# Kernel optimization log

Hardware: AMD Instinct MI355X
Metric: run time of the kernel (lower is better)

Reference implementation:

```python
import jax, jax.numpy as jnp
import numpy as np

CMP_STRIDE, CMP_BLOCK = 16, 32
SEL_BLOCK, SEL_COUNT = 64, 16
WINDOW = 512
B, S, HQ, HKV, D = 1, 1536, 16, 2, 128


def setup_inputs() -> dict:
    key = jax.random.key(0)
    ks = jax.random.split(key, 10)
    f = lambda k_, sh, sc=1.0: jax.random.normal(k_, sh, jnp.float32) * sc
    return {
        "q": f(ks[0], (B * S, HQ, D)),
        "k": f(ks[1], (B * S, HKV, D)),
        "v": f(ks[2], (B * S, HKV, D)),
        "Wk": f(ks[3], (CMP_BLOCK * D, D), 0.02),
        "bk": jnp.zeros((D,), jnp.float32),
        "Wv": f(ks[4], (CMP_BLOCK * D, D), 0.02),
        "bv": jnp.zeros((D,), jnp.float32),
        "pek": f(ks[5], (CMP_BLOCK, D), 0.02),
        "pev": f(ks[6], (CMP_BLOCK, D), 0.02),
        "Wg": f(ks[7], (D, 3), 0.02),
        "bg": jnp.zeros((3,), jnp.float32),
        "cu_seqlens": jnp.array([0, S], jnp.int32),
        "max_seqlen": S,
    }


def _compress(x, W, b, pe):
    # x: [B,T,H,D] -> overlapping blocks (stride 16, len 32) -> learned linear per block
    Bb, T, H, Dd = x.shape
    Tc = (T - CMP_BLOCK) // CMP_STRIDE + 1
    idx = jnp.arange(Tc)[:, None] * CMP_STRIDE + jnp.arange(CMP_BLOCK)[None, :]
    blk = x[:, idx] + pe[None, None, :, None, :]          # [B,Tc,L,H,D] + intra-block pos emb
    blk = blk.transpose(0, 1, 3, 2, 4).reshape(Bb, Tc, H, CMP_BLOCK * Dd)
    return blk @ W + b                                    # [B,Tc,H,D]


def _msoftmax(logits, mask):
    # masked softmax; fully-masked rows produce zeros
    logits = jnp.where(mask, logits, jnp.finfo(logits.dtype).min)
    m = jnp.max(logits, -1, keepdims=True)
    e = jnp.exp(logits - m) * mask
    return e / jnp.maximum(e.sum(-1, keepdims=True), 1e-9)


def _forward(q, k, v, Wk, bk, Wv, bv, pek, pev, Wg, bg):
    scale = 1.0 / jnp.sqrt(jnp.float32(D))
    G = HQ // HKV
    qb = q.reshape(B, S, HQ, D)
    kb = k.reshape(B, S, HKV, D)
    vb = v.reshape(B, S, HKV, D)
    pos = jnp.arange(S)[:, None]

    # ---- stage 1: compressed-KV attention ----
    ck = _compress(kb, Wk, bk, pek)                        # [B,Tc,HKV,D]
    cv = _compress(vb, Wv, bv, pev)
    Tc = ck.shape[1]
    ckh = jnp.repeat(ck, G, axis=2)
    cvh = jnp.repeat(cv, G, axis=2)
    cl = jnp.einsum('bshd,bthd->bhst', qb, ckh) * scale    # [B,HQ,S,Tc]
    cmask = (jnp.arange(Tc)[None, :] * CMP_STRIDE + CMP_BLOCK - 1) <= pos  # block fully visible
    cp = _msoftmax(cl, cmask[None, None])
    cmp_o = jnp.einsum('bhst,bthd->bshd', cp, cvh)

    # ---- stage 2: pooled-score top-k block selection ----
    score = cp.reshape(B, HKV, G, S, Tc).sum(2)            # sum over GQA group -> [B,HKV,S,Tc]
    Kp = SEL_BLOCK // CMP_STRIDE + 1                       # AvgPool1d kernel = 5
    St = SEL_BLOCK // CMP_STRIDE                           # stride = 4
    P = CMP_BLOCK // CMP_STRIDE - 2                        # padding = 0
    n_out = -(-(Tc + 2 * P - Kp) // St) + 1                # ceil_mode=True
    widx = jnp.arange(n_out)[:, None] * St - P + jnp.arange(Kp)[None, :]
    inb = (widx >= 0) & (widx < Tc)
    cnt = ((widx >= -P) & (widx < Tc + P)).sum(-1)         # count_include_pad divisor
    gathered = jnp.where(inb[None, None, None], score[..., jnp.clip(widx, 0, Tc - 1)], 0.0)
    pooled = gathered.sum(-1) / cnt                        # [B,HKV,S,n_out]
    _, top_idx = jax.lax.top_k(pooled, SEL_COUNT)          # [B,HKV,S,SEL_COUNT]

    # ---- stage 3: block-sparse selected attention + sliding window ----
    n_kblk = S // SEL_BLOCK
    blk_sel = (top_idx[..., None] == jnp.arange(n_kblk)).any(-2)   # [B,HKV,S,n_kblk]
    key_blk = jnp.arange(S) // SEL_BLOCK
    causal = jnp.arange(S)[None, :] <= pos                 # [S,S]
    sel_mask = jnp.take(blk_sel, key_blk, axis=-1) & causal[None, None]
    sel_mask = jnp.repeat(sel_mask, G, axis=1)             # [B,HQ,S,S]
    win_mask = causal & (jnp.arange(S)[None, :] > pos - WINDOW)

    kh = jnp.repeat(kb, G, axis=2)
    vh = jnp.repeat(vb, G, axis=2)
    logits = jnp.einsum('bshd,buhd->bhsu', qb, kh) * scale # [B,HQ,S,S]
    sel_o = jnp.einsum('bhsu,buhd->bshd', _msoftmax(logits, sel_mask), vh)
    win_o = jnp.einsum('bhsu,buhd->bshd', _msoftmax(logits, win_mask[None, None]), vh)

    # ---- gated combine of three branches ----
    gate = jax.nn.sigmoid(jnp.einsum('bshd,de->bshe', qb, Wg) + bg)  # [B,S,HQ,3]
    o = gate[..., 0:1] * sel_o + gate[..., 1:2] * win_o + gate[..., 2:3] * cmp_o
    return o.reshape(-1, HQ, D)


def reference(q, k, v, Wk, bk, Wv, bv, pek, pev, Wg, bg, cu_seqlens, max_seqlen):
    return _forward(q, k, v, Wk, bk, Wv, bv, pek, pev, Wg, bg)
```

## Files before the change

### kernel.cpp

```cpp
#include <hip/hip_runtime.h>


#define S_LEN 1536
#define HQ    16
#define HKV   2
#define DH    128
#define TC    95
#define WIN   512
#define TQ    16
#define SCALE 0.08838834764831845f

typedef _Float16 f16;
typedef f16   f16x4 __attribute__((ext_vector_type(4)));
typedef f16   f16x8 __attribute__((ext_vector_type(8)));
typedef float f32x4 __attribute__((ext_vector_type(4)));

__device__ inline f16x8 cvt8(float4 A, float4 B) {
    f16x8 h;
    h[0]=(f16)A.x; h[1]=(f16)A.y; h[2]=(f16)A.z; h[3]=(f16)A.w;
    h[4]=(f16)B.x; h[5]=(f16)B.y; h[6]=(f16)B.z; h[7]=(f16)B.w;
    return h;
}
__device__ inline f16x8 cvt8s(float4 A, float4 B, float s) {
    f16x8 h;
    h[0]=(f16)(A.x*s); h[1]=(f16)(A.y*s); h[2]=(f16)(A.z*s); h[3]=(f16)(A.w*s);
    h[4]=(f16)(B.x*s); h[5]=(f16)(B.y*s); h[6]=(f16)(B.z*s); h[7]=(f16)(B.w*s);
    return h;
}

__global__ __launch_bounds__(256) void compress_init_kernel(
    const float* __restrict__ bk, const float* __restrict__ bv,
    float* __restrict__ ck, float* __restrict__ cv)
{
    int i = blockIdx.x * 256 + threadIdx.x;
    int which = i >= TC*HKV*DH;
    int j = i - which*(TC*HKV*DH);
    int d = j & 127;
    (which ? cv : ck)[j] = (which ? bv : bk)[d];
}

__global__ __launch_bounds__(256) void compress_partial_kernel(
    const float* __restrict__ kin, const float* __restrict__ vin,
    const float* __restrict__ Wk,  const float* __restrict__ Wv,
    const float* __restrict__ pek, const float* __restrict__ pev,
    float* __restrict__ ck, float* __restrict__ cv)
{
    const int t0    = blockIdx.x * 5;
    const int kv    = blockIdx.y >> 1;
    const int which = blockIdx.y & 1;
    const int kc    = blockIdx.z;
    const float* __restrict__ x  = which ? vin : kin;
    const float* __restrict__ W  = which ? Wv  : Wk;
    const float* __restrict__ pe = which ? pev : pek;
    float* __restrict__ outp     = which ? cv  : ck;
    const int tid = threadIdx.x;
    const int hh  = tid >> 7;
    const int d   = tid & 127;

    __shared__ float xs[2][5][128];
    __shared__ float racc[5][128];
    float acc[5] = {0.f, 0.f, 0.f, 0.f, 0.f};

    #pragma unroll
    for (int il = 0; il < 2; ++il) {
        const int l = kc*4 + hh*2 + il;
        float p = pe[l*DH + d];
        #pragma unroll
        for (int tt = 0; tt < 5; ++tt) {
            int row = (t0 + tt)*16 + l;
            xs[hh][tt][d] = x[(row*HKV + kv)*DH + d] + p;
        }
        __syncthreads();
        const float* wcol = W + l*DH*DH + d;
        #pragma unroll 8
        for (int dd = 0; dd < 128; ++dd) {
            float wv = wcol[dd*DH];
            #pragma unroll
            for (int tt = 0; tt < 5; ++tt) acc[tt] += xs[hh][tt][dd] * wv;
        }
        __syncthreads();
    }
    if (hh == 1) {
        #pragma unroll
        for (int tt = 0; tt < 5; ++tt) racc[tt][d] = acc[tt];
    }
    __syncthreads();
    if (hh == 0) {
        #pragma unroll
        for (int tt = 0; tt < 5; ++tt)
            atomicAdd(&outp[((t0 + tt)*HKV + kv)*DH + d], acc[tt] + racc[tt][d]);
    }
}

__global__ __launch_bounds__(256) void cmp_attn_mfma(
    const float* __restrict__ q, const float* __restrict__ ck,
    const float* __restrict__ cv, float* __restrict__ cmp_o,
    unsigned int* __restrict__ blk_mask)
{
    const int s0   = blockIdx.x * 8;
    const int kv   = blockIdx.y;
    const int tid  = threadIdx.x;
    const int w    = tid >> 6;
    const int lane = tid & 63;
    const int quad = lane >> 4;
    const int l4   = lane & 15;

    __shared__ __align__(16) char BUF[52736];
    f16* __restrict__ CKH = (f16*)BUF;
    f16* __restrict__ CKL = (f16*)(BUF + 26112);
    f16* __restrict__ CVR = (f16*)BUF;
    f16* __restrict__ CVT = (f16*)(BUF + 26112);
    f16*   __restrict__ Pw = (f16*)BUF + w*1664;
    float* __restrict__ SC = (float*)(BUF + 13312);
    float* __restrict__ PO = (float*)(BUF + 16384);

    #pragma unroll
    for (int i = 0; i < 6; ++i) {
        int idx = i*256 + tid;
        int row = idx >> 4, cg = idx & 15;
        float4 A = make_float4(0.f,0.f,0.f,0.f), B = A;
        if (row < TC) {
            const float* src = ck + ((size_t)(row*HKV + kv))*DH + cg*8;
            A = *(const float4*)src; B = *(const float4*)(src + 4);
        }
        f16x8 h = cvt8(A, B);
        f16x8 l;
        l[0]=(f16)(A.x-(float)h[0]); l[1]=(f16)(A.y-(float)h[1]);
        l[2]=(f16)(A.z-(float)h[2]); l[3]=(f16)(A.w-(float)h[3]);
        l[4]=(f16)(B.x-(float)h[4]); l[5]=(f16)(B.y-(float)h[5]);
        l[6]=(f16)(B.z-(float)h[6]); l[7]=(f16)(B.w-(float)h[7]);
        *(f16x8*)&CKH[row*136 + cg*8] = h;
        *(f16x8*)&CKL[row*136 + cg*8] = l;
    }

    const int qrow_local = w*16 + l4;
    const int sA = s0 + (qrow_local >> 3);
    const int hA = qrow_local & 7;
    f16x8 aqh[4], aql[4];
    {
        const float* qrow = q + ((size_t)(sA*HQ + kv*8 + hA))*DH;
        #pragma unroll
        for (int ks = 0; ks < 4; ++ks) {
            float4 A = *(const float4*)(qrow + ks*32 + quad*8);
            float4 B = *(const float4*)(qrow + ks*32 + quad*8 + 4);
            A.x*=SCALE; A.y*=SCALE; A.z*=SCALE; A.w*=SCALE;
            B.x*=SCALE; B.y*=SCALE; B.z*=SCALE; B.w*=SCALE;
            f16x8 h = cvt8(A, B);
            f16x8 l;
            l[0]=(f16)(A.x-(float)h[0]); l[1]=(f16)(A.y-(float)h[1]);
            l[2]=(f16)(A.z-(float)h[2]); l[3]=(f16)(A.w-(float)h[3]);
            l[4]=(f16)(B.x-(float)h[4]); l[5]=(f16)(B.y-(float)h[5]);
            l[6]=(f16)(B.z-(float)h[6]); l[7]=(f16)(B.w-(float)h[7]);
            aqh[ks] = h; aql[ks] = l;
        }
    }
    __syncthreads();

    f32x4 sc[6];
    #pragma unroll
    for (int nt = 0; nt < 6; ++nt) {
        sc[nt] = (f32x4){0.f,0.f,0.f,0.f};
        #pragma unroll
        for (int ks = 0; ks < 4; ++ks) {
            f16x8 bh = *(const f16x8*)&CKH[(nt*16 + l4)*136 + ks*32 + quad*8];
            f16x8 bl = *(const f16x8*)&CKL[(nt*16 + l4)*136 + ks*32 + quad*8];
            sc[nt] = __builtin_amdgcn_mfma_f32_16x16x32_f16(aqh[ks], bh, sc[nt], 0, 0, 0);
            sc[nt] = __builtin_amdgcn_mfma_f32_16x16x32_f16(aql[ks], bh, sc[nt], 0, 0, 0);
            sc[nt] = __builtin_amdgcn_mfma_f32_16x16x32_f16(aqh[ks], bl, sc[nt], 0, 0, 0);
        }
    }
    __syncthreads();

    #pragma unroll
    for (int i = 0; i < 6; ++i) {
        int idx = i*256 + tid;
        int row = idx >> 4, cg = idx & 15;
        float4 A = make_float4(0.f,0.f,0.f,0.f), B = A;
        if (row < TC) {
            const float* src = cv + ((size_t)(row*HKV + kv))*DH + cg*8;
            A = *(const float4*)src; B = *(const float4*)(src + 4);
        }
        *(f16x8*)&CVR[row*136 + cg*8] = cvt8(A, B);
    }
    __syncthreads();
    #pragma unroll
    for (int i = 0; i < 6; ++i) {
        int idx = i*256 + tid;
        int d = idx & 127, tc = idx >> 7;
        f16x8 h;
        #pragma unroll
        for (int j = 0; j < 8; ++j) h[j] = CVR[(tc*8 + j)*136 + d];
        *(f16x8*)&CVT[d*104 + tc*8] = h;
    }
    __syncthreads();

    const int s_q = s0 + 2*w + (quad >> 1);
    const int nv  = (s_q >= 31) ? (((s_q - 31) >> 4) + 1) : 0;
    bool valid[6];
    #pragma unroll
    for (int nt = 0; nt < 6; ++nt) valid[nt] = (nt*16 + l4) < nv;

    float pn[6][4];
    float lsum[4];
    #pragma unroll
    for (int r = 0; r < 4; ++r) {
        float m = -3.4e38f;
        #pragma unroll
        for (int nt = 0; nt < 6; ++nt) m = fmaxf(m, valid[nt] ? sc[nt][r] : -3.4e38f);
        #pragma unroll
        for (int off = 1; off < 16; off <<= 1) m = fmaxf(m, __shfl_xor(m, off));
        float s = 0.f;
        #pragma unroll
        for (int nt = 0; nt < 6; ++nt) {
            float e = valid[nt] ? __expf(sc[nt][r] - m) : 0.f;
            pn[nt][r] = e;
            s += e;
        }
        #pragma unroll
        for (int off = 1; off < 16; off <<= 1) s += __shfl_xor(s, off);
        const float inv = 1.f / fmaxf(s, 1e-9f);
        #pragma unroll
        for (int nt = 0; nt < 6; ++nt) pn[nt][r] *= inv;
        lsum[r] = s;
    }
    (void)lsum;

    #pragma unroll
    for (int nt = 0; nt < 6; ++nt) {
        #pragma unroll
        for (int r = 0; r < 4; ++r)
            Pw[(quad*4 + r)*104 + nt*16 + l4] = (f16)pn[nt][r];
        float scq = pn[nt][0] + pn[nt][1] + pn[nt][2] + pn[nt][3];
        scq += __shfl_xor(scq, 16);
        if ((quad & 1) == 0)
            SC[(w*2 + (quad >> 1))*96 + nt*16 + l4] = scq;
    }

    {
        int qi = lane >> 5;
        int o  = lane & 31;
        bool sel = false;
        if (o < 24) {
            float acc = 0.f, cnt = 0.f;
            #pragma unroll
            for (int j = 0; j < 5; ++j) {
                int wd = o*4 + j;
                if (wd < TC) { acc += SC[(w*2 + qi)*96 + wd]; cnt += 1.f; }
            }
            PO[(w*2 + qi)*24 + o] = acc / cnt;
        }
        if (o < 24) {
            float pvv = PO[(w*2 + qi)*24 + o];
            int rank = 0;
            #pragma unroll
            for (int j = 0; j < 24; ++j) {
                float pj = PO[(w*2 + qi)*24 + j];
                rank += ((pj > pvv) || (pj == pvv && j < o)) ? 1 : 0;
            }
            sel = rank < 16;
        }
        unsigned long long b = __ballot(sel);
        if (lane == 0) {
            blk_mask[kv*S_LEN + s0 + 2*w]     = (unsigned int)(b & 0xFFFFFFull);
            blk_mask[kv*S_LEN + s0 + 2*w + 1] = (unsigned int)((b >> 32) & 0xFFFFFFull);
        }
    }

    f32x4 O[8];
    #pragma unroll
    for (int nf = 0; nf < 8; ++nf) O[nf] = (f32x4){0.f,0.f,0.f,0.f};
    #pragma unroll
    for (int ks2 = 0; ks2 < 3; ++ks2) {
        f16x8 ap = *(const f16x8*)&Pw[l4*104 + ks2*32 + quad*8];
        #pragma unroll
        for (int nf = 0; nf < 8; ++nf) {
            f16x8 bv = *(const f16x8*)&CVT[(nf*16 + l4)*104 + ks2*32 + quad*8];
            O[nf] = __builtin_amdgcn_mfma_f32_16x16x32_f16(ap, bv, O[nf], 0, 0, 0);
        }
    }
    #pragma unroll
    for (int r = 0; r < 4; ++r) {
        const int h_r = (quad & 1)*4 + r;
        const size_t base = ((size_t)(s_q*HQ + kv*8 + h_r))*DH;
        #pragma unroll
        for (int nf = 0; nf < 8; ++nf)
            cmp_o[base + nf*16 + l4] = O[nf][r];
    }
}

__global__ __launch_bounds__(256, 2) void main_attn_split(
    const float* __restrict__ q, const float* __restrict__ kg,
    const float* __restrict__ vg,
    const unsigned int* __restrict__ blk_mask,
    float* __restrict__ po, float* __restrict__ ml,
    int nsplit)
{
    const int t0    = (S_LEN/TQ - 1 - blockIdx.x) * TQ;
    const int kv    = blockIdx.y;
    const int z     = blockIdx.z & 1;
    const int split = blockIdx.z >> 1;
    const int tid   = threadIdx.x;
    const int w     = tid >> 6;
    const int lane  = tid & 63;
    const int quad  = lane >> 4;
    const int l4    = lane & 15;
    const int head  = z*4 + w;

    __shared__ __align__(16) f16 Klds[64*136];
    __shared__ __align__(16) f16 Vt[128*72];
    __shared__ __align__(16) f16 Plds[4][16*72];
    f16* __restrict__ Pw = Plds[w];

    int srow[4]; unsigned selm[4];
    #pragma unroll
    for (int r = 0; r < 4; ++r) {
        srow[r] = t0 + quad*4 + r;
        selm[r] = blk_mask[kv*S_LEN + srow[r]];
    }
    unsigned um = 0;
    for (int i = 0; i < TQ; ++i) um |= blk_mask[kv*S_LEN + t0 + i];

    const int nkb = ((t0 + TQ - 1) >> 6) + 1;
    const int wlo_tile = t0 - WIN + 1;

    unsigned act_all = 0;
    for (int kb2 = 0; kb2 < nkb; ++kb2) {
        bool a = ((um >> kb2) & 1u) || ((kb2*64 + 63) >= wlo_tile);
        if (a) act_all |= (1u << kb2);
    }
    unsigned act = 0;
    {
        int ii = 0;
        for (unsigned t = act_all; t; t &= t - 1, ++ii)
            if (ii % nsplit == split) act |= (t & -t);
    }
    if (act == 0) {
        #pragma unroll
        for (int r = 0; r < 4; ++r) {
            const size_t rh = (size_t)srow[r]*HQ + kv*8 + head;
            const size_t bs = ((size_t)(split*2+0)*S_LEN*HQ + rh)*DH;
            const size_t bw = ((size_t)(split*2+1)*S_LEN*HQ + rh)*DH;
            #pragma unroll
            for (int nf = 0; nf < 8; ++nf) {
                po[bs + nf*16 + l4] = 0.f;
                po[bw + nf*16 + l4] = 0.f;
            }
            if (l4 == 0) {
                const size_t ms = ((size_t)(split*2+0)*S_LEN*HQ + rh)*2;
                const size_t mw = ((size_t)(split*2+1)*S_LEN*HQ + rh)*2;
                ml[ms+0] = -1e30f; ml[ms+1] = 0.f;
                ml[mw+0] = -1e30f; ml[mw+1] = 0.f;
            }
        }
        return;
    }

    f16x8 aq[4];
    {
        const float* qrow = q + ((size_t)(t0 + l4)*HQ + kv*8 + head)*DH;
        #pragma unroll
        for (int ks = 0; ks < 4; ++ks) {
            float4 A = *(const float4*)(qrow + ks*32 + quad*8);
            float4 B = *(const float4*)(qrow + ks*32 + quad*8 + 4);
            aq[ks] = cvt8s(A, B, SCALE);
        }
    }

    f32x4 o_s[8], o_w[8];
    #pragma unroll
    for (int nf = 0; nf < 8; ++nf) {
        o_s[nf] = (f32x4){0.f,0.f,0.f,0.f};
        o_w[nf] = (f32x4){0.f,0.f,0.f,0.f};
    }
    float m_s[4], l_s[4], m_w[4], l_w[4];
    #pragma unroll
    for (int r = 0; r < 4; ++r) { m_s[r]=-1e30f; l_s[r]=0.f; m_w[r]=-1e30f; l_w[r]=0.f; }

    int key_[4], cg_[4], vd_[4], vk_[4];
    #pragma unroll
    for (int i = 0; i < 4; ++i) {
        int idx = i*256 + tid;
        key_[i] = idx >> 4;  cg_[i] = idx & 15;
        vd_[i]  = idx & 127; vk_[i] = idx >> 7;
    }

    float4 pkA[4], pkB[4];
    float  pv[4][8];
    int kb = __builtin_ctz(act); act &= act - 1;
    #pragma unroll
    for (int i = 0; i < 4; ++i) {
        const float* sK = kg + ((size_t)(kb*64 + key_[i])*HKV + kv)*DH + cg_[i]*8;
        pkA[i] = *(const float4*)sK; pkB[i] = *(const float4*)(sK + 4);
        #pragma unroll
        for (int j = 0; j < 8; ++j)
            pv[i][j] = vg[((size_t)(kb*64 + vk_[i]*8 + j)*HKV + kv)*DH + vd_[i]];
    }

    while (true) {
        __syncthreads();
        #pragma unroll
        for (int i = 0; i < 4; ++i)
            *(f16x8*)&Klds[key_[i]*136 + cg_[i]*8] = cvt8(pkA[i], pkB[i]);
        #pragma unroll
        for (int i = 0; i < 4; ++i) {
            f16x8 h;
            #pragma unroll
            for (int j = 0; j < 8; ++j) h[j] = (f16)pv[i][j];
            *(f16x8*)&Vt[vd_[i]*72 + vk_[i]*8] = h;
        }
        __syncthreads();

        const int cur = kb;
        const bool more = (act != 0);
        if (more) {
            kb = __builtin_ctz(act); act &= act - 1;
            #pragma unroll
            for (int i = 0; i < 4; ++i) {
                const float* sK = kg + ((size_t)(kb*64 + key_[i])*HKV + kv)*DH + cg_[i]*8;
                pkA[i] = *(const float4*)sK; pkB[i] = *(const float4*)(sK + 4);
                #pragma unroll
                for (int j = 0; j < 8; ++j)
                    pv[i][j] = vg[((size_t)(kb*64 + vk_[i]*8 + j)*HKV + kv)*DH + vd_[i]];
            }
        }

        f32x4 sc[4];
        #pragma unroll
        for (int nt = 0; nt < 4; ++nt) {
            sc[nt] = (f32x4){0.f,0.f,0.f,0.f};
            #pragma unroll
            for (int ks = 0; ks < 4; ++ks) {
                f16x8 bk = *(const f16x8*)&Klds[(nt*16 + l4)*136 + ks*32 + quad*8];
                sc[nt] = __builtin_amdgcn_mfma_f32_16x16x32_f16(aq[ks], bk, sc[nt], 0, 0, 0);
            }
        }

        const int keyb = cur*64;
        const bool any_sel = (um >> cur) & 1u;
        const bool any_win = (keyb + 63) >= wlo_tile;
        if (any_sel) {
            float rmax[4] = {-1e30f,-1e30f,-1e30f,-1e30f};
            #pragma unroll
            for (int nt = 0; nt < 4; ++nt) {
                int key = keyb + nt*16 + l4;
                #pragma unroll
                for (int r = 0; r < 4; ++r) {
                    bool ok = (key <= srow[r]) && ((selm[r] >> cur) & 1u);
                    rmax[r] = fmaxf(rmax[r], ok ? sc[nt][r] : -1e30f);
                }
            }
            float alpha[4];
            #pragma unroll
            for (int r = 0; r < 4; ++r) {
                #pragma unroll
                for (int off = 1; off < 16; off <<= 1)
                    rmax[r] = fmaxf(rmax[r], __shfl_xor(rmax[r], off));
                float nm = fmaxf(m_s[r], rmax[r]);
                alpha[r] = __expf(m_s[r] - nm);
                m_s[r] = nm;
            }
            float rs[4] = {0.f,0.f,0.f,0.f};
            #pragma unroll
            for (int nt = 0; nt < 4; ++nt) {
                int key = keyb + nt*16 + l4;
                #pragma unroll
                for (int r = 0; r < 4; ++r) {
                    bool ok = (key <= srow[r]) && ((selm[r] >> cur) & 1u);
                    float p = ok ? __expf(sc[nt][r] - m_s[r]) : 0.f;
                    rs[r] += p;
                    Pw[(quad*4 + r)*72 + nt*16 + l4] = (f16)p;
                }
            }
            #pragma unroll
            for (int r = 0; r < 4; ++r) {
                #pragma unroll
                for (int off = 1; off < 16; off <<= 1) rs[r] += __shfl_xor(rs[r], off);
                l_s[r] = l_s[r]*alpha[r] + rs[r];
            }
            #pragma unroll
            for (int nf = 0; nf < 8; ++nf) {
                #pragma unroll
                for (int r = 0; r < 4; ++r) o_s[nf][r] *= alpha[r];
            }
            #pragma unroll
            for (int ks2 = 0; ks2 < 2; ++ks2) {
                f16x8 ap = *(const f16x8*)&Pw[l4*72 + ks2*32 + quad*8];
                #pragma unroll
                for (int nf = 0; nf < 8; ++nf) {
                    f16x8 bv = *(const f16x8*)&Vt[(nf*16 + l4)*72 + ks2*32 + quad*8];
                    o_s[nf] = __builtin_amdgcn_mfma_f32_16x16x32_f16(ap, bv, o_s[nf], 0, 0, 0);
                }
            }
        }
        if (any_win) {
            float rmax[4] = {-1e30f,-1e30f,-1e30f,-1e30f};
            #pragma unroll
            for (int nt = 0; nt < 4; ++nt) {
                int key = keyb + nt*16 + l4;
                #pragma unroll
                for (int r = 0; r < 4; ++r) {
                    bool ok = (key <= srow[r]) && (key > srow[r] - WIN);
                    rmax[r] = fmaxf(rmax[r], ok ? sc[nt][r] : -1e30f);
                }
            }
            float alpha[4];
            #pragma unroll
            for (int r = 0; r < 4; ++r) {
                #pragma unroll
                for (int off = 1; off < 16; off <<= 1)
                    rmax[r] = fmaxf(rmax[r], __shfl_xor(rmax[r], off));
                float nm = fmaxf(m_w[r], rmax[r]);
                alpha[r] = __expf(m_w[r] - nm);
                m_w[r] = nm;
            }
            float rs[4] = {0.f,0.f,0.f,0.f};
            #pragma unroll
            for (int nt = 0; nt < 4; ++nt) {
                int key = keyb + nt*16 + l4;
                #pragma unroll
                for (int r = 0; r < 4; ++r) {
                    bool ok = (key <= srow[r]) && (key > srow[r] - WIN);
                    float p = ok ? __expf(sc[nt][r] - m_w[r]) : 0.f;
                    rs[r] += p;
                    Pw[(quad*4 + r)*72 + nt*16 + l4] = (f16)p;
                }
            }
            #pragma unroll
            for (int r = 0; r < 4; ++r) {
                #pragma unroll
                for (int off = 1; off < 16; off <<= 1) rs[r] += __shfl_xor(rs[r], off);
                l_w[r] = l_w[r]*alpha[r] + rs[r];
            }
            #pragma unroll
            for (int nf = 0; nf < 8; ++nf) {
                #pragma unroll
                for (int r = 0; r < 4; ++r) o_w[nf][r] *= alpha[r];
            }
            #pragma unroll
            for (int ks2 = 0; ks2 < 2; ++ks2) {
                f16x8 ap = *(const f16x8*)&Pw[l4*72 + ks2*32 + quad*8];
                #pragma unroll
                for (int nf = 0; nf < 8; ++nf) {
                    f16x8 bv = *(const f16x8*)&Vt[(nf*16 + l4)*72 + ks2*32 + quad*8];
                    o_w[nf] = __builtin_amdgcn_mfma_f32_16x16x32_f16(ap, bv, o_w[nf], 0, 0, 0);
                }
            }
        }

        if (!more) break;
    }

    #pragma unroll
    for (int r = 0; r < 4; ++r) {
        const size_t rh = (size_t)srow[r]*HQ + kv*8 + head;
        const size_t bs = ((size_t)(split*2+0)*S_LEN*HQ + rh)*DH;
        const size_t bw = ((size_t)(split*2+1)*S_LEN*HQ + rh)*DH;
        #pragma unroll
        for (int nf = 0; nf < 8; ++nf) {
            po[bs + nf*16 + l4] = o_s[nf][r];
            po[bw + nf*16 + l4] = o_w[nf][r];
        }
        if (l4 == 0) {
            const size_t ms = ((size_t)(split*2+0)*S_LEN*HQ + rh)*2;
            const size_t mw = ((size_t)(split*2+1)*S_LEN*HQ + rh)*2;
            ml[ms+0] = m_s[r]; ml[ms+1] = l_s[r];
            ml[mw+0] = m_w[r]; ml[mw+1] = l_w[r];
        }
    }
}

__global__ __launch_bounds__(256) void combine_kernel(
    const float* __restrict__ q, const float* __restrict__ po,
    const float* __restrict__ ml, const float* __restrict__ Wg,
    const float* __restrict__ bg, float* __restrict__ out, int nsplit)
{
    const int unit = blockIdx.x * 4 + (threadIdx.x >> 6);
    const int lane = threadIdx.x & 63;
    const int row  = unit >> 4;
    const int h    = unit & 15;
    const size_t rh = (size_t)row*HQ + h;

    float p0 = 0.f, p1 = 0.f, p2 = 0.f;
    const float* qrow = q + rh*DH;
    #pragma unroll
    for (int t = 0; t < 2; ++t) {
        int d = t*64 + lane;
        float qv = qrow[d];
        p0 += qv*Wg[d*3+0]; p1 += qv*Wg[d*3+1]; p2 += qv*Wg[d*3+2];
    }
    #pragma unroll
    for (int off = 1; off < 64; off <<= 1) {
        p0 += __shfl_xor(p0, off);
        p1 += __shfl_xor(p1, off);
        p2 += __shfl_xor(p2, off);
    }
    const float g0 = 1.f/(1.f + __expf(-(p0 + bg[0])));
    const float g1 = 1.f/(1.f + __expf(-(p1 + bg[1])));
    const float g2 = 1.f/(1.f + __expf(-(p2 + bg[2])));

    float res0 = 0.f, res1 = 0.f;
    #pragma unroll
    for (int b = 0; b < 2; ++b) {
        float M = -1e30f;
        for (int s = 0; s < nsplit; ++s)
            M = fmaxf(M, ml[((size_t)(s*2+b)*S_LEN*HQ + rh)*2 + 0]);
        float L = 0.f, osum0 = 0.f, osum1 = 0.f;
        for (int s = 0; s < nsplit; ++s) {
            const size_t mlb = ((size_t)(s*2+b)*S_LEN*HQ + rh)*2;
            const float wgt = __expf(ml[mlb+0] - M);
            L += ml[mlb+1] * wgt;
            const size_t ob = ((size_t)(s*2+b)*S_LEN*HQ + rh)*DH;
            osum0 += po[ob + lane]      * wgt;
            osum1 += po[ob + 64 + lane] * wgt;
        }
        const float inv = 1.f / fmaxf(L, 1e-9f);
        const float g = b ? g1 : g0;
        res0 += g * osum0 * inv;
        res1 += g * osum1 * inv;
    }
    const size_t ob = rh*DH;
    out[ob + lane]      = res0 + g2*out[ob + lane];
    out[ob + 64 + lane] = res1 + g2*out[ob + 64 + lane];
}

__global__ __launch_bounds__(256, 2) void main_attn_mfma(
    const float* __restrict__ q, const float* __restrict__ kg,
    const float* __restrict__ vg, const float* cmp_o,
    const unsigned int* __restrict__ blk_mask,
    const float* __restrict__ Wg, const float* __restrict__ bg,
    float* out)
{
    const int t0   = (S_LEN/TQ - 1 - blockIdx.x) * TQ;
    const int kv   = blockIdx.y;
    const int z    = blockIdx.z;
    const int tid  = threadIdx.x;
    const int w    = tid >> 6;
    const int lane = tid & 63;
    const int quad = lane >> 4;
    const int l4   = lane & 15;
    const int head = z*4 + w;

    __shared__ __align__(16) f16 Klds[64*136];
    __shared__ __align__(16) f16 Vrow[64*136];
    __shared__ __align__(16) f16 Vt[128*72];
    __shared__ __align__(16) f16 Plds[4][16*72];
    f16* __restrict__ Pw = Plds[w];

    f16x8 aq[4];
    {
        const float* qrow = q + ((size_t)(t0 + l4)*HQ + kv*8 + head)*DH;
        #pragma unroll
        for (int ks = 0; ks < 4; ++ks) {
            float4 A = *(const float4*)(qrow + ks*32 + quad*8);
            float4 B = *(const float4*)(qrow + ks*32 + quad*8 + 4);
            aq[ks] = cvt8s(A, B, SCALE);
        }
    }

    int srow[4]; unsigned selm[4];
    #pragma unroll
    for (int r = 0; r < 4; ++r) {
        srow[r] = t0 + quad*4 + r;
        selm[r] = blk_mask[kv*S_LEN + srow[r]];
    }
    unsigned um = 0;
    for (int i = 0; i < TQ; ++i) um |= blk_mask[kv*S_LEN + t0 + i];

    f32x4 o_s[8], o_w[8];
    #pragma unroll
    for (int nf = 0; nf < 8; ++nf) {
        o_s[nf] = (f32x4){0.f,0.f,0.f,0.f};
        o_w[nf] = (f32x4){0.f,0.f,0.f,0.f};
    }
    float m_s[4], l_s[4], m_w[4], l_w[4];
    #pragma unroll
    for (int r = 0; r < 4; ++r) { m_s[r]=-1e30f; l_s[r]=0.f; m_w[r]=-1e30f; l_w[r]=0.f; }

    const int nkb = ((t0 + TQ - 1) >> 6) + 1;
    const int wlo_tile = t0 - WIN + 1;

    unsigned act = 0;
    for (int kb2 = 0; kb2 < nkb; ++kb2) {
        bool a = ((um >> kb2) & 1u) || ((kb2*64 + 63) >= wlo_tile);
        if (a) act |= (1u << kb2);
    }

    int key_[4], cg_[4];
    #pragma unroll
    for (int i = 0; i < 4; ++i) { int idx = i*256 + tid; key_[i] = idx >> 4; cg_[i] = idx & 15; }

    float4 pkA[4], pkB[4], pvA[4], pvB[4];
    int kb = __builtin_ctz(act); act &= act - 1;
    #pragma unroll
    for (int i = 0; i < 4; ++i) {
        const float* sK = kg + ((size_t)(kb*64 + key_[i])*HKV + kv)*DH + cg_[i]*8;
        const float* sV = vg + ((size_t)(kb*64 + key_[i])*HKV + kv)*DH + cg_[i]*8;
        pkA[i] = *(const float4*)sK; pkB[i] = *(const float4*)(sK + 4);
        pvA[i] = *(const float4*)sV; pvB[i] = *(const float4*)(sV + 4);
    }

    while (true) {
        __syncthreads();
        #pragma unroll
        for (int i = 0; i < 4; ++i) {
            *(f16x8*)&Klds[key_[i]*136 + cg_[i]*8] = cvt8(pkA[i], pkB[i]);
            *(f16x8*)&Vrow[key_[i]*136 + cg_[i]*8] = cvt8(pvA[i], pvB[i]);
        }
        __syncthreads();

        const int cur = kb;
        const bool more = (act != 0);
        if (more) {
            kb = __builtin_ctz(act); act &= act - 1;
            #pragma unroll
            for (int i = 0; i < 4; ++i) {
                const float* sK = kg + ((size_t)(kb*64 + key_[i])*HKV + kv)*DH + cg_[i]*8;
                const float* sV = vg + ((size_t)(kb*64 + key_[i])*HKV + kv)*DH + cg_[i]*8;
                pkA[i] = *(const float4*)sK; pkB[i] = *(const float4*)(sK + 4);
                pvA[i] = *(const float4*)sV; pvB[i] = *(const float4*)(sV + 4);
            }
        }

        #pragma unroll
        for (int i = 0; i < 4; ++i) {
            int idx = i*256 + tid;
            int d = idx & 127, kg8 = idx >> 7;
            f16x8 h;
            #pragma unroll
            for (int j = 0; j < 8; ++j) h[j] = Vrow[(kg8*8 + j)*136 + d];
            *(f16x8*)&Vt[d*72 + kg8*8] = h;
        }
        __syncthreads();

        f32x4 sc[4];
        #pragma unroll
        for (int nt = 0; nt < 4; ++nt) {
            sc[nt] = (f32x4){0.f,0.f,0.f,0.f};
            #pragma unroll
            for (int ks = 0; ks < 4; ++ks) {
                f16x8 bk = *(const f16x8*)&Klds[(nt*16 + l4)*136 + ks*32 + quad*8];
                sc[nt] = __builtin_amdgcn_mfma_f32_16x16x32_f16(aq[ks], bk, sc[nt], 0, 0, 0);
            }
        }

        const int keyb = cur*64;
        const bool any_sel = (um >> cur) & 1u;
        const bool any_win = (keyb + 63) >= wlo_tile;
        if (any_sel) {
            float rmax[4] = {-1e30f,-1e30f,-1e30f,-1e30f};
            #pragma unroll
            for (int nt = 0; nt < 4; ++nt) {
                int key = keyb + nt*16 + l4;
                #pragma unroll
                for (int r = 0; r < 4; ++r) {
                    bool ok = (key <= srow[r]) && ((selm[r] >> cur) & 1u);
                    rmax[r] = fmaxf(rmax[r], ok ? sc[nt][r] : -1e30f);
                }
            }
            float alpha[4];
            #pragma unroll
            for (int r = 0; r < 4; ++r) {
                #pragma unroll
                for (int off = 1; off < 16; off <<= 1)
                    rmax[r] = fmaxf(rmax[r], __shfl_xor(rmax[r], off));
                float nm = fmaxf(m_s[r], rmax[r]);
                alpha[r] = __expf(m_s[r] - nm);
                m_s[r] = nm;
            }
            float rs[4] = {0.f,0.f,0.f,0.f};
            #pragma unroll
            for (int nt = 0; nt < 4; ++nt) {
                int key = keyb + nt*16 + l4;
                #pragma unroll
                for (int r = 0; r < 4; ++r) {
                    bool ok = (key <= srow[r]) && ((selm[r] >> cur) & 1u);
                    float p = ok ? __expf(sc[nt][r] - m_s[r]) : 0.f;
                    rs[r] += p;
                    Pw[(quad*4 + r)*72 + nt*16 + l4] = (f16)p;
                }
            }
            #pragma unroll
            for (int r = 0; r < 4; ++r) {
                #pragma unroll
                for (int off = 1; off < 16; off <<= 1) rs[r] += __shfl_xor(rs[r], off);
                l_s[r] = l_s[r]*alpha[r] + rs[r];
            }
            #pragma unroll
            for (int nf = 0; nf < 8; ++nf) {
                #pragma unroll
                for (int r = 0; r < 4; ++r) o_s[nf][r] *= alpha[r];
            }
            #pragma unroll
            for (int ks2 = 0; ks2 < 2; ++ks2) {
                f16x8 ap = *(const f16x8*)&Pw[l4*72 + ks2*32 + quad*8];
                #pragma unroll
                for (int nf = 0; nf < 8; ++nf) {
                    f16x8 bv = *(const f16x8*)&Vt[(nf*16 + l4)*72 + ks2*32 + quad*8];
                    o_s[nf] = __builtin_amdgcn_mfma_f32_16x16x32_f16(ap, bv, o_s[nf], 0, 0, 0);
                }
            }
        }
        if (any_win) {
            float rmax[4] = {-1e30f,-1e30f,-1e30f,-1e30f};
            #pragma unroll
            for (int nt = 0; nt < 4; ++nt) {
                int key = keyb + nt*16 + l4;
                #pragma unroll
                for (int r = 0; r < 4; ++r) {
                    bool ok = (key <= srow[r]) && (key > srow[r] - WIN);
                    rmax[r] = fmaxf(rmax[r], ok ? sc[nt][r] : -1e30f);
                }
            }
            float alpha[4];
            #pragma unroll
            for (int r = 0; r < 4; ++r) {
                #pragma unroll
                for (int off = 1; off < 16; off <<= 1)
                    rmax[r] = fmaxf(rmax[r], __shfl_xor(rmax[r], off));
                float nm = fmaxf(m_w[r], rmax[r]);
                alpha[r] = __expf(m_w[r] - nm);
                m_w[r] = nm;
            }
            float rs[4] = {0.f,0.f,0.f,0.f};
            #pragma unroll
            for (int nt = 0; nt < 4; ++nt) {
                int key = keyb + nt*16 + l4;
                #pragma unroll
                for (int r = 0; r < 4; ++r) {
                    bool ok = (key <= srow[r]) && (key > srow[r] - WIN);
                    float p = ok ? __expf(sc[nt][r] - m_w[r]) : 0.f;
                    rs[r] += p;
                    Pw[(quad*4 + r)*72 + nt*16 + l4] = (f16)p;
                }
            }
            #pragma unroll
            for (int r = 0; r < 4; ++r) {
                #pragma unroll
                for (int off = 1; off < 16; off <<= 1) rs[r] += __shfl_xor(rs[r], off);
                l_w[r] = l_w[r]*alpha[r] + rs[r];
            }
            #pragma unroll
            for (int nf = 0; nf < 8; ++nf) {
                #pragma unroll
                for (int r = 0; r < 4; ++r) o_w[nf][r] *= alpha[r];
            }
            #pragma unroll
            for (int ks2 = 0; ks2 < 2; ++ks2) {
                f16x8 ap = *(const f16x8*)&Pw[l4*72 + ks2*32 + quad*8];
                #pragma unroll
                for (int nf = 0; nf < 8; ++nf) {
                    f16x8 bv = *(const f16x8*)&Vt[(nf*16 + l4)*72 + ks2*32 + quad*8];
                    o_w[nf] = __builtin_amdgcn_mfma_f32_16x16x32_f16(ap, bv, o_w[nf], 0, 0, 0);
                }
            }
        }

        if (!more) break;
    }

    float inv_s[4], inv_w[4];
    #pragma unroll
    for (int r = 0; r < 4; ++r) {
        inv_s[r] = 1.f / fmaxf(l_s[r], 1e-9f);
        inv_w[r] = 1.f / fmaxf(l_w[r], 1e-9f);
    }
    float gt[4][3];
    #pragma unroll
    for (int r = 0; r < 4; ++r) {
        float p0 = 0.f, p1 = 0.f, p2 = 0.f;
        const float* qrow = q + ((size_t)srow[r]*HQ + kv*8 + head)*DH + l4*8;
        #pragma unroll
        for (int j = 0; j < 8; ++j) {
            float qv = qrow[j];
            int d = l4*8 + j;
            p0 += qv * Wg[d*3 + 0];
            p1 += qv * Wg[d*3 + 1];
            p2 += qv * Wg[d*3 + 2];
        }
        #pragma unroll
        for (int off = 1; off < 16; off <<= 1) {
            p0 += __shfl_xor(p0, off);
            p1 += __shfl_xor(p1, off);
            p2 += __shfl_xor(p2, off);
        }
        gt[r][0] = 1.f/(1.f + __expf(-(p0 + bg[0])));
        gt[r][1] = 1.f/(1.f + __expf(-(p1 + bg[1])));
        gt[r][2] = 1.f/(1.f + __expf(-(p2 + bg[2])));
    }
    #pragma unroll
    for (int nf = 0; nf < 8; ++nf) {
        int d = nf*16 + l4;
        #pragma unroll
        for (int r = 0; r < 4; ++r) {
            size_t oi = ((size_t)srow[r]*HQ + kv*8 + head)*DH + d;
            float cm = cmp_o[oi];
            out[oi] = gt[r][0]*o_s[nf][r]*inv_s[r]
                    + gt[r][1]*o_w[nf][r]*inv_w[r]
                    + gt[r][2]*cm;
        }
    }
}

extern "C" void kernel_launch(void* const* d_in, const int* in_sizes, int n_in,
                              void* d_out, int out_size, void* d_ws, size_t ws_size,
                              hipStream_t stream) {
    const float* q   = (const float*)d_in[0];
    const float* k   = (const float*)d_in[1];
    const float* v   = (const float*)d_in[2];
    const float* Wk  = (const float*)d_in[3];
    const float* bk  = (const float*)d_in[4];
    const float* Wv  = (const float*)d_in[5];
    const float* bv  = (const float*)d_in[6];
    const float* pek = (const float*)d_in[7];
    const float* pev = (const float*)d_in[8];
    const float* Wg  = (const float*)d_in[9];
    const float* bg  = (const float*)d_in[10];
    float* out = (float*)d_out;

    char* ws = (char*)d_ws;
    float* ck = (float*)ws;
    float* cv = (float*)(ws + 98304);
    unsigned int* blk_mask = (unsigned int*)(ws + 196608);
    float* cmp_o = out;

    compress_init_kernel<<<dim3(190), 256, 0, stream>>>(bk, bv, ck, cv);
    compress_partial_kernel<<<dim3(19, 4, 8), 256, 0, stream>>>(
        k, v, Wk, Wv, pek, pev, ck, cv);
    cmp_attn_mfma<<<dim3(S_LEN/8, HKV), 256, 0, stream>>>(
        q, ck, cv, cmp_o, blk_mask);

    const size_t base      = 208896;
    const size_t o_per_sp  = (size_t)2 * S_LEN * HQ * DH * 4;
    const size_t ml_per_sp = (size_t)2 * S_LEN * HQ * 2 * 4;
    const size_t per_split = o_per_sp + ml_per_sp;

    int nsplit = 0;
    if (ws_size >= base + 3*per_split)      nsplit = 3;
    else if (ws_size >= base + 2*per_split) nsplit = 2;

    if (nsplit >= 2) {
        float* po  = (float*)(ws + base);
        float* mlb = (float*)(ws + base + (size_t)nsplit * o_per_sp);
        main_attn_split<<<dim3(S_LEN/TQ, HKV, 2*nsplit), 256, 0, stream>>>(
            q, k, v, blk_mask, po, mlb, nsplit);
        combine_kernel<<<dim3(S_LEN*HQ/4), 256, 0, stream>>>(
            q, po, mlb, Wg, bg, out, nsplit);
    } else {
        main_attn_mfma<<<dim3(S_LEN/TQ, HKV, 2), 256, 0, stream>>>(
            q, k, v, cmp_o, blk_mask, Wg, bg, out);
    }
}
```

Before: 221.1 us.

## Use lazy online-softmax rescaling with threshold and deferred row-sum reductions

Initialises the running max to a fixed value and skips the max shuffle-reduction and output rescaling unless some lane's local tile max exceeds the running max by a threshold. The per-tile row-sum shuffle reduction is replaced by per-lane partial sums reduced once after the loop. Selected and window probabilities now go to separate LDS buffers so both can be computed before either PV MFMA. This cuts cross-lane shuffles and exp/rescale work per key tile, at the cost of extra LDS and a risk of fp16 overflow or precision loss in P when scores stay below the threshold but well above the running max.

```diff
diff --git a/kernel.cpp b/kernel.cpp
--- a/kernel.cpp
+++ b/kernel.cpp
@@ -9,6 +9,8 @@
 #define WIN   512
 #define TQ    16
 #define SCALE 0.08838834764831845f
+#define M_INIT 4.0f
+#define THR    8.0f
 
 typedef _Float16 f16;
 typedef f16   f16x4 __attribute__((ext_vector_type(4)));
@@ -308,8 +310,10 @@
 
     __shared__ __align__(16) f16 Klds[64*136];
     __shared__ __align__(16) f16 Vt[128*72];
-    __shared__ __align__(16) f16 Plds[4][16*72];
-    f16* __restrict__ Pw = Plds[w];
+    __shared__ __align__(16) f16 PldsS[4][16*72];
+    __shared__ __align__(16) f16 PldsW[4][16*72];
+    f16* __restrict__ PwS = PldsS[w];
+    f16* __restrict__ PwW = PldsW[w];
 
     int srow[4]; unsigned selm[4];
     #pragma unroll
@@ -374,7 +378,7 @@
     }
     float m_s[4], l_s[4], m_w[4], l_w[4];
     #pragma unroll
-    for (int r = 0; r < 4; ++r) { m_s[r]=-1e30f; l_s[r]=0.f; m_w[r]=-1e30f; l_w[r]=0.f; }
+    for (int r = 0; r < 4; ++r) { m_s[r]=M_INIT; l_s[r]=0.f; m_w[r]=M_INIT; l_w[r]=0.f; }
 
     int key_[4], cg_[4], vd_[4], vk_[4];
     #pragma unroll
@@ -438,53 +442,98 @@
         const int keyb = cur*64;
         const bool any_sel = (um >> cur) & 1u;
         const bool any_win = (keyb + 63) >= wlo_tile;
+        unsigned selb[4];
+        #pragma unroll
+        for (int r = 0; r < 4; ++r) selb[r] = (selm[r] >> cur) & 1u;
+
+        float lmx_s[4] = {-1e30f,-1e30f,-1e30f,-1e30f};
+        float lmx_w[4] = {-1e30f,-1e30f,-1e30f,-1e30f};
+        #pragma unroll
+        for (int nt = 0; nt < 4; ++nt) {
+            int key = keyb + nt*16 + l4;
+            #pragma unroll
+            for (int r = 0; r < 4; ++r) {
+                bool okc = key <= srow[r];
+                bool okS = okc && selb[r];
+                bool okW = okc && (key > srow[r] - WIN);
+                lmx_s[r] = fmaxf(lmx_s[r], okS ? sc[nt][r] : -1e30f);
+                lmx_w[r] = fmaxf(lmx_w[r], okW ? sc[nt][r] : -1e30f);
+            }
+        }
+
+        bool cond = true;
         if (any_sel) {
-            float rmax[4] = {-1e30f,-1e30f,-1e30f,-1e30f};
+            #pragma unroll
+            for (int r = 0; r < 4; ++r) cond = cond && (lmx_s[r] <= m_s[r] + THR);
+        }
+        if (any_win) {
+            #pragma unroll
+            for (int r = 0; r < 4; ++r) cond = cond && (lmx_w[r] <= m_w[r] + THR);
+        }
+        if (!__all(cond)) {
+            if (any_sel) {
+                #pragma unroll
+                for (int r = 0; r < 4; ++r) {
+                    float rm = lmx_s[r];
+                    #pragma unroll
+                    for (int off = 1; off < 16; off <<= 1)
+                        rm = fmaxf(rm, __shfl_xor(rm, off));
+                    float nm = fmaxf(m_s[r], rm);
+                    float alpha = __expf(m_s[r] - nm);
+                    m_s[r] = nm;
+                    l_s[r] *= alpha;
+                    #pragma unroll
+                    for (int nf = 0; nf < 8; ++nf) o_s[nf][r] *= alpha;
+                }
+            }
+            if (any_win) {
+                #pragma unroll
+                for (int r = 0; r < 4; ++r) {
+                    float rm = lmx_w[r];
+                    #pragma unroll
+                    for (int off = 1; off < 16; off <<= 1)
+                        rm = fmaxf(rm, __shfl_xor(rm, off));
+                    float nm = fmaxf(m_w[r], rm);
+                    float alpha = __expf(m_w[r] - nm);
+                    m_w[r] = nm;
+                    l_w[r] *= alpha;
+                    #pragma unroll
+                    for (int nf = 0; nf < 8; ++nf) o_w[nf][r] *= alpha;
+                }
+            }
+        }
+
+        if (any_sel) {
             #pragma unroll
             for (int nt = 0; nt < 4; ++nt) {
                 int key = keyb + nt*16 + l4;
                 #pragma unroll
                 for (int r = 0; r < 4; ++r) {
-                    bool ok = (key <= srow[r]) && ((selm[r] >> cur) & 1u);
-                    rmax[r] = fmaxf(rmax[r], ok ? sc[nt][r] : -1e30f);
-                }
-            }
-            float alpha[4];
-            #pragma unroll
-            for (int r = 0; r < 4; ++r) {
-                #pragma unroll
-                for (int off = 1; off < 16; off <<= 1)
-                    rmax[r] = fmaxf(rmax[r], __shfl_xor(rmax[r], off));
-                float nm = fmaxf(m_s[r], rmax[r]);
-                alpha[r] = __expf(m_s[r] - nm);
-                m_s[r] = nm;
-            }
-            float rs[4] = {0.f,0.f,0.f,0.f};
+                    bool ok = (key <= srow[r]) && selb[r];
+                    float p = ok ? __expf(sc[nt][r] - m_s[r]) : 0.f;
+                    l_s[r] += p;
+                    PwS[(quad*4 + r)*72 + nt*16 + l4] = (f16)p;
+                }
+            }
+        }
+        if (any_win) {
             #pragma unroll
             for (int nt = 0; nt < 4; ++nt) {
                 int key = keyb + nt*16 + l4;
                 #pragma unroll
                 for (int r = 0; r < 4; ++r) {
-                    bool ok = (key <= srow[r]) && ((selm[r] >> cur) & 1u);
-                    float p = ok ? __expf(sc[nt][r] - m_s[r]) : 0.f;
-                    rs[r] += p;
-                    Pw[(quad*4 + r)*72 + nt*16 + l4] = (f16)p;
-                }
-            }
-            #pragma unroll
-            for (int r = 0; r < 4; ++r) {
-                #pragma unroll
-                for (int off = 1; off < 16; off <<= 1) rs[r] += __shfl_xor(rs[r], off);
-                l_s[r] = l_s[r]*alpha[r] + rs[r];
-            }
-            #pragma unroll
-            for (int nf = 0; nf < 8; ++nf) {
-                #pragma unroll
-                for (int r = 0; r < 4; ++r) o_s[nf][r] *= alpha[r];
-            }
+                    bool ok = (key <= srow[r]) && (key > srow[r] - WIN);
+                    float p = ok ? __expf(sc[nt][r] - m_w[r]) : 0.f;
+                    l_w[r] += p;
+                    PwW[(quad*4 + r)*72 + nt*16 + l4] = (f16)p;
+                }
+            }
+        }
+
+        if (any_sel) {
             #pragma unroll
             for (int ks2 = 0; ks2 < 2; ++ks2) {
-                f16x8 ap = *(const f16x8*)&Pw[l4*72 + ks2*32 + quad*8];
+                f16x8 ap = *(const f16x8*)&PwS[l4*72 + ks2*32 + quad*8];
                 #pragma unroll
                 for (int nf = 0; nf < 8; ++nf) {
                     f16x8 bv = *(const f16x8*)&Vt[(nf*16 + l4)*72 + ks2*32 + quad*8];
@@ -493,52 +542,9 @@
             }
         }
         if (any_win) {
-            float rmax[4] = {-1e30f,-1e30f,-1e30f,-1e30f};
-            #pragma unroll
-            for (int nt = 0; nt < 4; ++nt) {
-                int key = keyb + nt*16 + l4;
-                #pragma unroll
-                for (int r = 0; r < 4; ++r) {
-                    bool ok = (key <= srow[r]) && (key > srow[r] - WIN);
-                    rmax[r] = fmaxf(rmax[r], ok ? sc[nt][r] : -1e30f);
-                }
-            }
-            float alpha[4];
-            #pragma unroll
-            for (int r = 0; r < 4; ++r) {
-                #pragma unroll
-                for (int off = 1; off < 16; off <<= 1)
-                    rmax[r] = fmaxf(rmax[r], __shfl_xor(rmax[r], off));
-                float nm = fmaxf(m_w[r], rmax[r]);
-                alpha[r] = __expf(m_w[r] - nm);
-                m_w[r] = nm;
-            }
-            float rs[4] = {0.f,0.f,0.f,0.f};
-            #pragma unroll
-            for (int nt = 0; nt < 4; ++nt) {
-                int key = keyb + nt*16 + l4;
-                #pragma unroll
-                for (int r = 0; r < 4; ++r) {
-                    bool ok = (key <= srow[r]) && (key > srow[r] - WIN);
-                    float p = ok ? __expf(sc[nt][r] - m_w[r]) : 0.f;
-                    rs[r] += p;
-                    Pw[(quad*4 + r)*72 + nt*16 + l4] = (f16)p;
-                }
-            }
-            #pragma unroll
-            for (int r = 0; r < 4; ++r) {
-                #pragma unroll
-                for (int off = 1; off < 16; off <<= 1) rs[r] += __shfl_xor(rs[r], off);
-                l_w[r] = l_w[r]*alpha[r] + rs[r];
-            }
-            #pragma unroll
-            for (int nf = 0; nf < 8; ++nf) {
-                #pragma unroll
-                for (int r = 0; r < 4; ++r) o_w[nf][r] *= alpha[r];
-            }
             #pragma unroll
             for (int ks2 = 0; ks2 < 2; ++ks2) {
-                f16x8 ap = *(const f16x8*)&Pw[l4*72 + ks2*32 + quad*8];
+                f16x8 ap = *(const f16x8*)&PwW[l4*72 + ks2*32 + quad*8];
                 #pragma unroll
                 for (int nf = 0; nf < 8; ++nf) {
                     f16x8 bv = *(const f16x8*)&Vt[(nf*16 + l4)*72 + ks2*32 + quad*8];
@@ -548,6 +554,15 @@
         }
 
         if (!more) break;
+    }
+
+    #pragma unroll
+    for (int r = 0; r < 4; ++r) {
+        #pragma unroll
+        for (int off = 1; off < 16; off <<= 1) {
+            l_s[r] += __shfl_xor(l_s[r], off);
+            l_w[r] += __shfl_xor(l_w[r], off);
+        }
     }
 
     #pragma unroll
```

Measured after the change: 200.9 us. 9.1% less time.
